# Kernel optimization log

Measured on AMD Instinct MI355X. Metric: run time of the kernel, lower is better.

Reference implementation:

```python
import jax, jax.numpy as jnp
import numpy as np

S, B, D, H = 512, 16, 512, 8  # seq_len, batch, d_model, n_heads
DH = D // H


def setup_inputs() -> dict:
    key = jax.random.key(0)
    k1, k2, k3, k4, k5 = jax.random.split(key, 5)
    x = jax.random.normal(k1, (S, B, D), dtype=jnp.float32)
    # nn.MultiheadAttention params: packed in_proj [3D, D], out_proj [D, D]
    W_in = jax.random.normal(k2, (3 * D, D), dtype=jnp.float32) * (D ** -0.5)
    b_in = jax.random.normal(k3, (3 * D,), dtype=jnp.float32) * 0.02
    W_out = jax.random.normal(k4, (D, D), dtype=jnp.float32) * (D ** -0.5)
    b_out = jax.random.normal(k5, (D,), dtype=jnp.float32) * 0.02
    return {"x": x, "W_in": W_in, "b_in": b_in, "W_out": W_out, "b_out": b_out}


def _mha(q_in, k_in, v_in, W_in, b_in, W_out, b_out):
    """torch.nn.MultiheadAttention (batch_first=False, eval mode). Inputs: (S, B, D)."""
    Wq, Wk, Wv = jnp.split(W_in, 3, axis=0)
    bq, bk, bv = jnp.split(b_in, 3)

    def heads(t):  # (S, B, D) -> (B, H, S, DH)
        s, b, _ = t.shape
        return t.reshape(s, b, H, DH).transpose(1, 2, 0, 3)

    q = heads(q_in @ Wq.T + bq) * (DH ** -0.5)
    k = heads(k_in @ Wk.T + bk)
    v = heads(v_in @ Wv.T + bv)
    attn = jax.nn.softmax(jnp.einsum('bhsd,bhtd->bhst', q, k), axis=-1)
    o = jnp.einsum('bhst,bhtd->bhsd', attn, v)          # (B, H, S, DH)
    o = o.transpose(2, 0, 1, 3).reshape(q_in.shape)      # (S, B, D)
    return o @ W_out.T + b_out


def reference(x, W_in, b_in, W_out, b_out):
    ch = jnp.arange(x.shape[-1])  # channel indices of last dim

    def step(acc, i):
        # x_i: only channel i kept (mirrors x_i[..., i] = x[..., i])
        x_i = jnp.where(ch == i, x, 0.0)
        # x_i_prime = where(x_i == 0, x, 0): x with channel i zeroed (where nonzero)
        x_ip = jnp.where(x_i == 0.0, x, 0.0)
        out = _mha(x_i, x_ip, x_ip, W_in, b_in, W_out, b_out)
        return acc + out, None

    # loop runs x.size(1) times, exactly as the torch code
    acc, _ = jax.lax.scan(step, jnp.zeros_like(x), jnp.arange(x.shape[1]))
    return acc
```

## Files before the change

### kernel.cpp

```cpp
#include <hip/hip_runtime.h>

#define S_LEN 512
#define BATCH 16
#define DMODEL 512
#define NHEAD 8
#define DH 64
#define NI 16

typedef float f32x4 __attribute__((ext_vector_type(4)));
typedef float f32x2 __attribute__((ext_vector_type(2)));
typedef short s16x8 __attribute__((ext_vector_type(8)));

__device__ __forceinline__ unsigned short f2bf(float f){
  unsigned int u = __float_as_uint(f);
  u += 0x7FFFu + ((u >> 16) & 1u);
  return (unsigned short)(u >> 16);
}

__device__ __forceinline__ void async16(const unsigned short* g, unsigned short* l){
  __builtin_amdgcn_global_load_lds(
      (const __attribute__((address_space(1))) unsigned int*)g,
      (__attribute__((address_space(3))) unsigned int*)l, 16, 0, 0);
}

template<int CTRL>
__device__ __forceinline__ float dppAdd(float x){
  int v = __builtin_amdgcn_update_dpp(0, __float_as_int(x), CTRL, 0xF, 0xF, true);
  return x + __int_as_float(v);
}

__global__ void k_prep(const float* __restrict__ x, unsigned short* __restrict__ xb,
                       float* __restrict__ zcol){
  int bidx = blockIdx.x;
  if (bidx < 4096){
    int t = bidx * 256 + threadIdx.x;
    float4 v = reinterpret_cast<const float4*>(x)[t];
    ushort4 o;
    o.x = f2bf(v.x); o.y = f2bf(v.y); o.z = f2bf(v.z); o.w = f2bf(v.w);
    reinterpret_cast<ushort4*>(xb)[t] = o;
  } else {
    int tid = (bidx - 4096) * 256 + threadIdx.x;
    int t = tid & 511; int bi = tid >> 9; int b = bi >> 4; int i = bi & 15;
    zcol[tid] = x[(size_t)(t * BATCH + b) * DMODEL + i];
  }
}

__global__ void k_wcvt(const float* __restrict__ Win, const float* __restrict__ Wout,
                       unsigned short* __restrict__ Winb, unsigned short* __restrict__ Wob){
  int bidx = blockIdx.x;
  if (bidx < 768){
    int t = bidx * 256 + threadIdx.x;
    float4 v = reinterpret_cast<const float4*>(Win)[t];
    ushort4 o;
    o.x = f2bf(v.x); o.y = f2bf(v.y); o.z = f2bf(v.z); o.w = f2bf(v.w);
    reinterpret_cast<ushort4*>(Winb)[t] = o;
  } else {
    int t = (bidx - 768) * 256 + threadIdx.x;
    float4 v = reinterpret_cast<const float4*>(Wout)[t];
    ushort4 o;
    o.x = f2bf(v.x); o.y = f2bf(v.y); o.z = f2bf(v.z); o.w = f2bf(v.w);
    reinterpret_cast<ushort4*>(Wob)[t] = o;
  }
}

__global__ __launch_bounds__(256) void k_kv2(const unsigned short* __restrict__ xb,
    const unsigned short* __restrict__ Winb, const float* __restrict__ b_in,
    float* __restrict__ Kf, unsigned short* __restrict__ Vfb){
  __shared__ unsigned short As[2][128 * 32];
  __shared__ unsigned short Bs[2][128 * 32];
  int tid = threadIdx.x;
  int w = tid >> 6, l = tid & 63;
  int ln = l & 15, kb = l >> 4;
  int wr = w >> 1, wc = w & 1;
  int m0 = blockIdx.x * 128;
  int n0 = blockIdx.y * 128;
  const unsigned short* Brow = Winb + (size_t)512 * DMODEL;

  f32x4 acc[4][4];
  #pragma unroll
  for (int mi = 0; mi < 4; ++mi)
    #pragma unroll
    for (int nj = 0; nj < 4; ++nj) acc[mi][nj] = (f32x4){0.f,0.f,0.f,0.f};

  int c0 = tid, c1 = 256 + tid;
  int r0 = c0 >> 2, q0 = c0 & 3, r1 = c1 >> 2, q1 = c1 & 3;
  int lb0 = (w * 64) * 8, lb1 = (256 + w * 64) * 8;

  #define STAGE_KV(kt, buf) do { int k0 = (kt) * 32;                                   \
    async16(xb   + (size_t)(m0 + r0) * DMODEL + k0 + q0 * 8, &As[buf][lb0]);           \
    async16(xb   + (size_t)(m0 + r1) * DMODEL + k0 + q1 * 8, &As[buf][lb1]);           \
    async16(Brow + (size_t)(n0 + r0) * DMODEL + k0 + q0 * 8, &Bs[buf][lb0]);           \
    async16(Brow + (size_t)(n0 + r1) * DMODEL + k0 + q1 * 8, &Bs[buf][lb1]);           \
  } while(0)

  STAGE_KV(0, 0);
  __syncthreads();
  int cur = 0;
  for (int kt = 0; kt < 16; ++kt){
    if (kt < 15) STAGE_KV(kt + 1, cur ^ 1);
    const unsigned short* Ab = &As[cur][(wr * 64 + ln) * 32 + kb * 8];
    const unsigned short* Bb = &Bs[cur][(wc * 64 + ln) * 32 + kb * 8];
    s16x8 af[4], bf[4];
    #pragma unroll
    for (int mi = 0; mi < 4; ++mi) af[mi] = *reinterpret_cast<const s16x8*>(Ab + mi * 16 * 32);
    #pragma unroll
    for (int nj = 0; nj < 4; ++nj) bf[nj] = *reinterpret_cast<const s16x8*>(Bb + nj * 16 * 32);
    #pragma unroll
    for (int mi = 0; mi < 4; ++mi)
      #pragma unroll
      for (int nj = 0; nj < 4; ++nj)
        acc[mi][nj] = __builtin_amdgcn_mfma_f32_16x16x32_bf16(af[mi], bf[nj], acc[mi][nj], 0, 0, 0);
    __syncthreads();
    cur ^= 1;
  }
  #undef STAGE_KV

  #pragma unroll
  for (int nj = 0; nj < 4; ++nj){
    int n = n0 + wc * 64 + nj * 16 + ln;
    float bias = b_in[512 + n];
    #pragma unroll
    for (int mi = 0; mi < 4; ++mi){
      #pragma unroll
      for (int r = 0; r < 4; ++r){
        int m = m0 + wr * 64 + mi * 16 + kb * 4 + r;
        float v = acc[mi][nj][r] + bias;
        if (n < DMODEL) Kf[(size_t)m * DMODEL + n] = v;
        else            Vfb[(size_t)m * DMODEL + (n - DMODEL)] = f2bf(v);
      }
    }
  }
}

__global__ void k_tr(const unsigned short* __restrict__ Vfb, unsigned short* __restrict__ VfT){
  __shared__ unsigned short tile[32][34];
  int b = blockIdx.z; int t0 = blockIdx.x * 32; int d0 = blockIdx.y * 32;
  int tx = threadIdx.x & 31, ty = threadIdx.x >> 5;
  #pragma unroll
  for (int k = 0; k < 4; ++k){
    int row = ty + 8 * k;
    tile[row][tx] = Vfb[(size_t)((t0 + row) * BATCH + b) * DMODEL + d0 + tx];
  }
  __syncthreads();
  #pragma unroll
  for (int k = 0; k < 4; ++k){
    int row = ty + 8 * k;
    VfT[(size_t)b * (DMODEL * S_LEN) + (size_t)(d0 + row) * S_LEN + t0 + tx] = tile[tx][row];
  }
}

__global__ __launch_bounds__(512) void k_gh(const float* __restrict__ W_in,
    const float* __restrict__ b_in, const float* __restrict__ Kf,
    const float* __restrict__ zcol, float* __restrict__ G, float* __restrict__ H){
  const float SCALE = 0.18033688011112042f;
  int bh = blockIdx.x; int b = bh >> 3, h = bh & 7;
  __shared__ float u[64][17];
  __shared__ float cvec[64];
  __shared__ float alpha[16], beta[16];
  int tid = threadIdx.x;
  for (int idx = tid; idx < 1024; idx += 512){
    int d = idx >> 4, i = idx & 15;
    u[d][i] = W_in[(size_t)(h * 64 + d) * DMODEL + i];
  }
  if (tid < 64) cvec[tid] = b_in[h * 64 + tid];
  __syncthreads();
  if (tid < 16){
    float a = 0.f, be = 0.f;
    for (int d = 0; d < 64; ++d){
      float wk = W_in[(size_t)(512 + h * 64 + d) * DMODEL + tid];
      a  += u[d][tid] * wk;
      be += cvec[d] * wk;
    }
    alpha[tid] = a; beta[tid] = be;
  }
  __syncthreads();
  int t = tid;
  float K[64];
  const float* kp = Kf + (size_t)(t * BATCH + b) * DMODEL + h * 64;
  #pragma unroll
  for (int d = 0; d < 64; d += 4){
    float4 v = *reinterpret_cast<const float4*>(kp + d);
    K[d] = v.x; K[d+1] = v.y; K[d+2] = v.z; K[d+3] = v.w;
  }
  float Bt = 0.f;
  #pragma unroll
  for (int d = 0; d < 64; ++d) Bt += cvec[d] * K[d];
  for (int i = 0; i < 16; ++i){
    float A = 0.f;
    #pragma unroll
    for (int d = 0; d < 64; ++d) A += u[d][i] * K[d];
    float z = zcol[(size_t)(b * 16 + i) * 512 + t];
    G[(size_t)(bh * 16 + i) * 512 + t] = (A  - alpha[i] * z) * SCALE;
    H[(size_t)(bh * 16 + i) * 512 + t] = (Bt - beta[i]  * z) * SCALE;
  }
}

__global__ __launch_bounds__(512) void k_smpv(const float* __restrict__ G,
    const float* __restrict__ H, const float* __restrict__ zcol,
    const unsigned short* __restrict__ VfT, const float* __restrict__ W_in,
    unsigned short* __restrict__ Ob){
  __shared__ unsigned short Pl[32 * 512];
  __shared__ float Rs[32][17];
  __shared__ float Wvl[64][17];
  int j = blockIdx.x;
  int xcd = j & 7, rest = j >> 3;
  int bh_hi = rest & 15, sb = rest >> 4;
  int bh = bh_hi * 8 + xcd;
  int b = bh >> 3, h = bh & 7;
  int tid = threadIdx.x, w = tid >> 6, l = tid & 63;

  for (int idx = tid; idx < 1024; idx += 512){
    int d = idx >> 4, i = idx & 15;
    Wvl[d][i] = W_in[(size_t)(2 * DMODEL + h * 64 + d) * DMODEL + i];
  }

  const float* gb = G    + ((size_t)bh * NI) * S_LEN;
  const float* hb = H    + ((size_t)bh * NI) * S_LEN;
  const float* zb = zcol + ((size_t)b  * NI) * S_LEN;
  int t0 = l * 4, t1 = 256 + l * 4;
  int s_w = sb * 32 + w * 4;

  f32x2 Pacc[4][4];
  #pragma unroll
  for (int r = 0; r < 4; ++r)
    #pragma unroll
    for (int jp = 0; jp < 4; ++jp) Pacc[r][jp] = (f32x2){0.f, 0.f};

  for (int i = 0; i < NI; ++i){
    const float* gp = gb + (i << 9);
    const float* hp = hb + (i << 9);
    const float* zp = zb + (i << 9);
    f32x4 gA = *reinterpret_cast<const f32x4*>(gp + t0);
    f32x4 gB = *reinterpret_cast<const f32x4*>(gp + t1);
    f32x4 hA = *reinterpret_cast<const f32x4*>(hp + t0);
    f32x4 hB = *reinterpret_cast<const f32x4*>(hp + t1);
    f32x4 zA = *reinterpret_cast<const f32x4*>(zp + t0);
    f32x4 zB = *reinterpret_cast<const f32x4*>(zp + t1);
    float4 y4 = *reinterpret_cast<const float4*>(zp + s_w);
    f32x2 g2[4] = {gA.lo, gA.hi, gB.lo, gB.hi};
    f32x2 h2[4] = {hA.lo, hA.hi, hB.lo, hB.hi};
    f32x2 z2[4] = {zA.lo, zA.hi, zB.lo, zB.hi};
    float ys[4] = {y4.x, y4.y, y4.z, y4.w};

    f32x2 E[4][4];
    float pd[4], pr[4];
    #pragma unroll
    for (int r = 0; r < 4; ++r){
      f32x2 yv = {ys[r], ys[r]};
      f32x2 dacc = {0.f, 0.f}, racc = {0.f, 0.f};
      #pragma unroll
      for (int jp = 0; jp < 4; ++jp){
        f32x2 a = yv * g2[jp] + h2[jp];
        f32x2 e;
        e.x = __builtin_amdgcn_exp2f(a.x);
        e.y = __builtin_amdgcn_exp2f(a.y);
        E[r][jp] = e;
        dacc += e;
        racc += e * z2[jp];
      }
      pd[r] = dacc.x + dacc.y;
      pr[r] = racc.x + racc.y;
    }

    bool b5 = (l & 32) != 0, b4 = (l & 16) != 0;
    float dk0 = b5 ? pd[2] : pd[0], dv0 = b5 ? pd[0] : pd[2];
    float dk1 = b5 ? pd[3] : pd[1], dv1 = b5 ? pd[1] : pd[3];
    float rk0 = b5 ? pr[2] : pr[0], rv0 = b5 ? pr[0] : pr[2];
    float rk1 = b5 ? pr[3] : pr[1], rv1 = b5 ? pr[1] : pr[3];
    float dq0 = dk0 + __shfl_xor(dv0, 32);
    float dq1 = dk1 + __shfl_xor(dv1, 32);
    float rq0 = rk0 + __shfl_xor(rv0, 32);
    float rq1 = rk1 + __shfl_xor(rv1, 32);
    float dkk = b4 ? dq1 : dq0, dss = b4 ? dq0 : dq1;
    float rkk = b4 ? rq1 : rq0, rss = b4 ? rq0 : rq1;
    float du = dkk + __shfl_xor(dss, 16);
    float ru = rkk + __shfl_xor(rss, 16);
    du = dppAdd<0x140>(du); ru = dppAdd<0x140>(ru);
    du = dppAdd<0x141>(du); ru = dppAdd<0x141>(ru);
    du = dppAdd<0x4E>(du);  ru = dppAdd<0x4E>(ru);
    du = dppAdd<0xB1>(du);  ru = dppAdd<0xB1>(ru);
    float inv = __builtin_amdgcn_rcpf(du);
    if ((l & 15) == 0)
      Rs[w * 4 + (l >> 4)][i] = ru * inv;
    #pragma unroll
    for (int r = 0; r < 4; ++r){
      float ir = __int_as_float(__builtin_amdgcn_readlane(__float_as_int(inv), 16 * r));
      f32x2 iv = {ir, ir};
      #pragma unroll
      for (int jp = 0; jp < 4; ++jp) Pacc[r][jp] += E[r][jp] * iv;
    }
  }

  #pragma unroll
  for (int r = 0; r < 4; ++r){
    int sl = w * 4 + r;
    unsigned int u0 = (unsigned int)f2bf(Pacc[r][0].x) | ((unsigned int)f2bf(Pacc[r][0].y) << 16);
    unsigned int u1 = (unsigned int)f2bf(Pacc[r][1].x) | ((unsigned int)f2bf(Pacc[r][1].y) << 16);
    unsigned int u2 = (unsigned int)f2bf(Pacc[r][2].x) | ((unsigned int)f2bf(Pacc[r][2].y) << 16);
    unsigned int u3 = (unsigned int)f2bf(Pacc[r][3].x) | ((unsigned int)f2bf(Pacc[r][3].y) << 16);
    int xr = (sl & 7) << 4;
    char* rowp = (char*)Pl + sl * 1024;
    uint2 v01; v01.x = u0; v01.y = u1;
    uint2 v23; v23.x = u2; v23.y = u3;
    *reinterpret_cast<uint2*>(rowp + ((l * 8) ^ xr)) = v01;
    *reinterpret_cast<uint2*>(rowp + ((512 + l * 8) ^ xr)) = v23;
  }
  __syncthreads();

  int ln = l & 15, kb = l >> 4;
  int sh = (w & 1) * 16;
  int dt = (w >> 1) * 16;
  const unsigned short* bp = VfT + (size_t)b * (DMODEL * S_LEN)
                             + (size_t)(h * 64 + dt + ln) * S_LEN + kb * 8;
  char* arow = (char*)Pl + (sh + ln) * 1024;
  int xa = (ln & 7) << 4;
  f32x4 acc = {0.f, 0.f, 0.f, 0.f};
  #pragma unroll
  for (int kt = 0; kt < 16; ++kt){
    s16x8 af = *reinterpret_cast<const s16x8*>(arow + ((kt * 64 + kb * 16) ^ xa));
    s16x8 bf = *reinterpret_cast<const s16x8*>(bp + kt * 32);
    acc = __builtin_amdgcn_mfma_f32_16x16x32_bf16(af, bf, acc, 0, 0, 0);
  }
  #pragma unroll
  for (int r = 0; r < 4; ++r){
    int sl = sh + kb * 4 + r;
    float corr = 0.f;
    #pragma unroll
    for (int i = 0; i < 16; ++i) corr += Rs[sl][i] * Wvl[dt + ln][i];
    float v = acc[r] - corr;
    int m = sb * 32 + sl;
    Ob[(size_t)(m * BATCH + b) * DMODEL + h * 64 + dt + ln] = f2bf(v);
  }
}

__global__ __launch_bounds__(256) void k_out2(const unsigned short* __restrict__ Ob,
    const unsigned short* __restrict__ Wob, const float* __restrict__ b_out,
    float* __restrict__ out){
  __shared__ unsigned short As[2][128 * 32];
  __shared__ unsigned short Bs[2][128 * 32];
  int tid = threadIdx.x;
  int w = tid >> 6, l = tid & 63;
  int ln = l & 15, kb = l >> 4;
  int wr = w >> 1, wc = w & 1;
  int m0 = blockIdx.x * 128;
  int n0 = blockIdx.y * 128;

  f32x4 acc[4][4];
  #pragma unroll
  for (int mi = 0; mi < 4; ++mi)
    #pragma unroll
    for (int nj = 0; nj < 4; ++nj) acc[mi][nj] = (f32x4){0.f,0.f,0.f,0.f};

  int c0 = tid, c1 = 256 + tid;
  int r0 = c0 >> 2, q0 = c0 & 3, r1 = c1 >> 2, q1 = c1 & 3;
  int lb0 = (w * 64) * 8, lb1 = (256 + w * 64) * 8;

  #define STAGE_O(kt, buf) do { int k0 = (kt) * 32;                                    \
    async16(Ob  + (size_t)(m0 + r0) * DMODEL + k0 + q0 * 8, &As[buf][lb0]);            \
    async16(Ob  + (size_t)(m0 + r1) * DMODEL + k0 + q1 * 8, &As[buf][lb1]);            \
    async16(Wob + (size_t)(n0 + r0) * DMODEL + k0 + q0 * 8, &Bs[buf][lb0]);            \
    async16(Wob + (size_t)(n0 + r1) * DMODEL + k0 + q1 * 8, &Bs[buf][lb1]);            \
  } while(0)

  STAGE_O(0, 0);
  __syncthreads();
  int cur = 0;
  for (int kt = 0; kt < 16; ++kt){
    if (kt < 15) STAGE_O(kt + 1, cur ^ 1);
    const unsigned short* Ab = &As[cur][(wr * 64 + ln) * 32 + kb * 8];
    const unsigned short* Bb = &Bs[cur][(wc * 64 + ln) * 32 + kb * 8];
    s16x8 af[4], bf[4];
    #pragma unroll
    for (int mi = 0; mi < 4; ++mi) af[mi] = *reinterpret_cast<const s16x8*>(Ab + mi * 16 * 32);
    #pragma unroll
    for (int nj = 0; nj < 4; ++nj) bf[nj] = *reinterpret_cast<const s16x8*>(Bb + nj * 16 * 32);
    #pragma unroll
    for (int mi = 0; mi < 4; ++mi)
      #pragma unroll
      for (int nj = 0; nj < 4; ++nj)
        acc[mi][nj] = __builtin_amdgcn_mfma_f32_16x16x32_bf16(af[mi], bf[nj], acc[mi][nj], 0, 0, 0);
    __syncthreads();
    cur ^= 1;
  }
  #undef STAGE_O

  #pragma unroll
  for (int nj = 0; nj < 4; ++nj){
    int n = n0 + wc * 64 + nj * 16 + ln;
    float bias = 16.0f * b_out[n];
    #pragma unroll
    for (int mi = 0; mi < 4; ++mi){
      #pragma unroll
      for (int r = 0; r < 4; ++r){
        int m = m0 + wr * 64 + mi * 16 + kb * 4 + r;
        out[(size_t)m * DMODEL + n] = acc[mi][nj][r] + bias;
      }
    }
  }
}

extern "C" void kernel_launch(void* const* d_in, const int* in_sizes, int n_in,
                              void* d_out, int out_size, void* d_ws, size_t ws_size,
                              hipStream_t stream) {
  const float* x     = (const float*)d_in[0];
  const float* W_in  = (const float*)d_in[1];
  const float* b_in  = (const float*)d_in[2];
  const float* W_out = (const float*)d_in[3];
  const float* b_out = (const float*)d_in[4];
  float* out = (float*)d_out;

  size_t off = 0;
  char* base = (char*)d_ws;
  auto alloc = [&](size_t bytes) -> void* {
    void* p = base + off;
    off += (bytes + 255) & ~(size_t)255;
    return p;
  };
  unsigned short* xb   = (unsigned short*)alloc(8388608);
  unsigned short* Winb = (unsigned short*)alloc(1572864);
  unsigned short* Wob  = (unsigned short*)alloc(524288);
  float*          zcol = (float*)alloc(524288);
  float*          Kf   = (float*)alloc(16777216);
  unsigned short* Vfb  = (unsigned short*)alloc(8388608);
  unsigned short* VfT  = (unsigned short*)alloc(8388608);
  float*          G    = (float*)alloc(4194304);
  float*          H    = (float*)alloc(4194304);
  unsigned short* Ob   = (unsigned short*)alloc(8388608);

  k_prep<<<4608, 256, 0, stream>>>(x, xb, zcol);
  k_wcvt<<<1024, 256, 0, stream>>>(W_in, W_out, Winb, Wob);

  { dim3 g(64, 8); k_kv2<<<g, 256, 0, stream>>>(xb, Winb, b_in, Kf, Vfb); }
  { dim3 g(16, 16, 16); k_tr<<<g, 256, 0, stream>>>(Vfb, VfT); }
  k_gh<<<128, 512, 0, stream>>>(W_in, b_in, Kf, zcol, G, H);

  k_smpv<<<2048, 512, 0, stream>>>(G, H, zcol, VfT, W_in, Ob);

  { dim3 g(64, 4); k_out2<<<g, 256, 0, stream>>>(Ob, Wob, b_out, out); }
}
```

Before: 186.6 us.

## Software-pipeline G/H/z loads in k_smpv and fuse zcol extraction into x conversion

The k_smpv inner loop over the 16 channel indices is restructured so each iteration's global loads are issued one step ahead of its compute, using two register sets, to hide load latency behind the exp2 work. The cross-lane reduction is rewritten with symmetric shuffles, and launch bounds now request 3 blocks per multiprocessor, which caps register use. k_prep writes zcol from the same float4 it already converts, which removes the separate strided-gather blocks. Double-buffering raises register pressure, and the occupancy hint could force spills.

New measurement: 214.4 us. 1.15x slower.

```diff
diff --git a/kernel.cpp b/kernel.cpp
--- a/kernel.cpp
+++ b/kernel.cpp
@@ -31,17 +31,19 @@
 
 __global__ void k_prep(const float* __restrict__ x, unsigned short* __restrict__ xb,
                        float* __restrict__ zcol){
-  int bidx = blockIdx.x;
-  if (bidx < 4096){
-    int t = bidx * 256 + threadIdx.x;
-    float4 v = reinterpret_cast<const float4*>(x)[t];
-    ushort4 o;
-    o.x = f2bf(v.x); o.y = f2bf(v.y); o.z = f2bf(v.z); o.w = f2bf(v.w);
-    reinterpret_cast<ushort4*>(xb)[t] = o;
-  } else {
-    int tid = (bidx - 4096) * 256 + threadIdx.x;
-    int t = tid & 511; int bi = tid >> 9; int b = bi >> 4; int i = bi & 15;
-    zcol[tid] = x[(size_t)(t * BATCH + b) * DMODEL + i];
+  int tid = blockIdx.x * 256 + threadIdx.x;
+  float4 v = reinterpret_cast<const float4*>(x)[tid];
+  ushort4 o;
+  o.x = f2bf(v.x); o.y = f2bf(v.y); o.z = f2bf(v.z); o.w = f2bf(v.w);
+  reinterpret_cast<ushort4*>(xb)[tid] = o;
+  int d0 = (tid & 127) * 4;
+  if (d0 < 16){
+    int row = tid >> 7;
+    int t = row >> 4, b = row & 15;
+    zcol[(size_t)(b * 16 + d0 + 0) * 512 + t] = v.x;
+    zcol[(size_t)(b * 16 + d0 + 1) * 512 + t] = v.y;
+    zcol[(size_t)(b * 16 + d0 + 2) * 512 + t] = v.z;
+    zcol[(size_t)(b * 16 + d0 + 3) * 512 + t] = v.w;
   }
 }
 
@@ -195,7 +197,7 @@
   }
 }
 
-__global__ __launch_bounds__(512) void k_smpv(const float* __restrict__ G,
+__global__ __launch_bounds__(512, 3) void k_smpv(const float* __restrict__ G,
     const float* __restrict__ H, const float* __restrict__ zcol,
     const unsigned short* __restrict__ VfT, const float* __restrict__ W_in,
     unsigned short* __restrict__ Ob){
@@ -226,70 +228,89 @@
     #pragma unroll
     for (int jp = 0; jp < 4; ++jp) Pacc[r][jp] = (f32x2){0.f, 0.f};
 
-  for (int i = 0; i < NI; ++i){
-    const float* gp = gb + (i << 9);
-    const float* hp = hb + (i << 9);
-    const float* zp = zb + (i << 9);
-    f32x4 gA = *reinterpret_cast<const f32x4*>(gp + t0);
-    f32x4 gB = *reinterpret_cast<const f32x4*>(gp + t1);
-    f32x4 hA = *reinterpret_cast<const f32x4*>(hp + t0);
-    f32x4 hB = *reinterpret_cast<const f32x4*>(hp + t1);
-    f32x4 zA = *reinterpret_cast<const f32x4*>(zp + t0);
-    f32x4 zB = *reinterpret_cast<const f32x4*>(zp + t1);
-    float4 y4 = *reinterpret_cast<const float4*>(zp + s_w);
-    f32x2 g2[4] = {gA.lo, gA.hi, gB.lo, gB.hi};
-    f32x2 h2[4] = {hA.lo, hA.hi, hB.lo, hB.hi};
-    f32x2 z2[4] = {zA.lo, zA.hi, zB.lo, zB.hi};
-    float ys[4] = {y4.x, y4.y, y4.z, y4.w};
-
-    f32x2 E[4][4];
-    float pd[4], pr[4];
-    #pragma unroll
-    for (int r = 0; r < 4; ++r){
-      f32x2 yv = {ys[r], ys[r]};
-      f32x2 dacc = {0.f, 0.f}, racc = {0.f, 0.f};
-      #pragma unroll
-      for (int jp = 0; jp < 4; ++jp){
-        f32x2 a = yv * g2[jp] + h2[jp];
-        f32x2 e;
-        e.x = __builtin_amdgcn_exp2f(a.x);
-        e.y = __builtin_amdgcn_exp2f(a.y);
-        E[r][jp] = e;
-        dacc += e;
-        racc += e * z2[jp];
-      }
-      pd[r] = dacc.x + dacc.y;
-      pr[r] = racc.x + racc.y;
-    }
-
-    bool b5 = (l & 32) != 0, b4 = (l & 16) != 0;
-    float dk0 = b5 ? pd[2] : pd[0], dv0 = b5 ? pd[0] : pd[2];
-    float dk1 = b5 ? pd[3] : pd[1], dv1 = b5 ? pd[1] : pd[3];
-    float rk0 = b5 ? pr[2] : pr[0], rv0 = b5 ? pr[0] : pr[2];
-    float rk1 = b5 ? pr[3] : pr[1], rv1 = b5 ? pr[1] : pr[3];
-    float dq0 = dk0 + __shfl_xor(dv0, 32);
-    float dq1 = dk1 + __shfl_xor(dv1, 32);
-    float rq0 = rk0 + __shfl_xor(rv0, 32);
-    float rq1 = rk1 + __shfl_xor(rv1, 32);
-    float dkk = b4 ? dq1 : dq0, dss = b4 ? dq0 : dq1;
-    float rkk = b4 ? rq1 : rq0, rss = b4 ? rq0 : rq1;
-    float du = dkk + __shfl_xor(dss, 16);
-    float ru = rkk + __shfl_xor(rss, 16);
-    du = dppAdd<0x140>(du); ru = dppAdd<0x140>(ru);
-    du = dppAdd<0x141>(du); ru = dppAdd<0x141>(ru);
-    du = dppAdd<0x4E>(du);  ru = dppAdd<0x4E>(ru);
-    du = dppAdd<0xB1>(du);  ru = dppAdd<0xB1>(ru);
-    float inv = __builtin_amdgcn_rcpf(du);
-    if ((l & 15) == 0)
-      Rs[w * 4 + (l >> 4)][i] = ru * inv;
-    #pragma unroll
-    for (int r = 0; r < 4; ++r){
-      float ir = __int_as_float(__builtin_amdgcn_readlane(__float_as_int(inv), 16 * r));
-      f32x2 iv = {ir, ir};
-      #pragma unroll
-      for (int jp = 0; jp < 4; ++jp) Pacc[r][jp] += E[r][jp] * iv;
-    }
-  }
+  bool b5 = (l & 32) != 0, b4 = (l & 16) != 0;
+
+  f32x4 ga0, gc0, ha0, hc0, za0, zc0; float4 yy0;
+  f32x4 ga1, gc1, ha1, hc1, za1, zc1; float4 yy1;
+
+  #define LOADI(S, ii) do { int _o = ((ii) << 9);                          \
+    ga##S = *reinterpret_cast<const f32x4*>(gb + _o + t0);                 \
+    gc##S = *reinterpret_cast<const f32x4*>(gb + _o + t1);                 \
+    ha##S = *reinterpret_cast<const f32x4*>(hb + _o + t0);                 \
+    hc##S = *reinterpret_cast<const f32x4*>(hb + _o + t1);                 \
+    za##S = *reinterpret_cast<const f32x4*>(zb + _o + t0);                 \
+    zc##S = *reinterpret_cast<const f32x4*>(zb + _o + t1);                 \
+    yy##S = *reinterpret_cast<const float4*>(zb + _o + s_w);               \
+  } while(0)
+
+  #define COMPUTE(S, ii) do {                                                       \
+    f32x2 g2[4] = {ga##S.lo, ga##S.hi, gc##S.lo, gc##S.hi};                         \
+    f32x2 h2[4] = {ha##S.lo, ha##S.hi, hc##S.lo, hc##S.hi};                         \
+    f32x2 z2[4] = {za##S.lo, za##S.hi, zc##S.lo, zc##S.hi};                         \
+    float ys[4] = {yy##S.x, yy##S.y, yy##S.z, yy##S.w};                             \
+    f32x2 E[4][4];                                                                  \
+    float pd[4], pr[4];                                                             \
+    _Pragma("unroll")                                                               \
+    for (int r = 0; r < 4; ++r){                                                    \
+      f32x2 yv = {ys[r], ys[r]};                                                    \
+      f32x2 dacc = {0.f, 0.f}, racc = {0.f, 0.f};                                   \
+      _Pragma("unroll")                                                             \
+      for (int jp = 0; jp < 4; ++jp){                                               \
+        f32x2 a = yv * g2[jp] + h2[jp];                                             \
+        f32x2 e;                                                                    \
+        e.x = __builtin_amdgcn_exp2f(a.x);                                          \
+        e.y = __builtin_amdgcn_exp2f(a.y);                                          \
+        E[r][jp] = e;                                                               \
+        dacc += e;                                                                  \
+        racc += e * z2[jp];                                                         \
+      }                                                                             \
+      pd[r] = dacc.x + dacc.y;                                                      \
+      pr[r] = racc.x + racc.y;                                                      \
+    }                                                                               \
+                    \
+    float s0d = pd[0] + __shfl_xor(pd[0], 32);                                      \
+    float s2d = pd[2] + __shfl_xor(pd[2], 32);                                      \
+    float s1d = pd[1] + __shfl_xor(pd[1], 32);                                      \
+    float s3d = pd[3] + __shfl_xor(pd[3], 32);                                      \
+    float s0r = pr[0] + __shfl_xor(pr[0], 32);                                      \
+    float s2r = pr[2] + __shfl_xor(pr[2], 32);                                      \
+    float s1r = pr[1] + __shfl_xor(pr[1], 32);                                      \
+    float s3r = pr[3] + __shfl_xor(pr[3], 32);                                      \
+    float dq0 = b5 ? s2d : s0d;                                                     \
+    float dq1 = b5 ? s3d : s1d;                                                     \
+    float rq0 = b5 ? s2r : s0r;                                                     \
+    float rq1 = b5 ? s3r : s1r;                                                     \
+    float dd0 = dq0 + __shfl_xor(dq0, 16);                                          \
+    float dd1 = dq1 + __shfl_xor(dq1, 16);                                          \
+    float rr0 = rq0 + __shfl_xor(rq0, 16);                                          \
+    float rr1 = rq1 + __shfl_xor(rq1, 16);                                          \
+    float du = b4 ? dd1 : dd0;                                                      \
+    float ru = b4 ? rr1 : rr0;                                                      \
+    du = dppAdd<0x140>(du); ru = dppAdd<0x140>(ru);                                 \
+    du = dppAdd<0x141>(du); ru = dppAdd<0x141>(ru);                                 \
+    du = dppAdd<0x4E>(du);  ru = dppAdd<0x4E>(ru);                                  \
+    du = dppAdd<0xB1>(du);  ru = dppAdd<0xB1>(ru);                                  \
+    float inv = __builtin_amdgcn_rcpf(du);                                          \
+    if ((l & 15) == 0)                                                              \
+      Rs[w * 4 + (l >> 4)][ii] = ru * inv;                                          \
+    _Pragma("unroll")                                                               \
+    for (int r = 0; r < 4; ++r){                                                    \
+      float ir = __int_as_float(__builtin_amdgcn_readlane(__float_as_int(inv), 16 * r)); \
+      f32x2 iv = {ir, ir};                                                          \
+      _Pragma("unroll")                                                             \
+      for (int jp = 0; jp < 4; ++jp) Pacc[r][jp] += E[r][jp] * iv;                  \
+    }                                                                               \
+  } while(0)
+
+  LOADI(0, 0);
+  for (int i = 0; i < NI; i += 2){
+    LOADI(1, i + 1);
+    COMPUTE(0, i);
+    if (i + 2 < NI) LOADI(0, i + 2);
+    COMPUTE(1, i + 1);
+  }
+  #undef LOADI
+  #undef COMPUTE
 
   #pragma unroll
   for (int r = 0; r < 4; ++r){
@@ -427,7 +448,7 @@
   float*          H    = (float*)alloc(4194304);
   unsigned short* Ob   = (unsigned short*)alloc(8388608);
 
-  k_prep<<<4608, 256, 0, stream>>>(x, xb, zcol);
+  k_prep<<<4096, 256, 0, stream>>>(x, xb, zcol);
   k_wcvt<<<1024, 256, 0, stream>>>(W_in, W_out, Winb, Wob);
 
   { dim3 g(64, 8); k_kv2<<<g, 256, 0, stream>>>(xb, Winb, b_in, Kf, Vfb); }
```
